# Performance work log

Measured on AMD Instinct MI355X. Metric: run time of the kernel, lower is better.

The kernel has to match this reference:

```python
import jax, jax.numpy as jnp
import numpy as np

D = 384      # d_model
H = 6        # num_heads
K = 8        # k_neighbors
B = 8        # batch
N = 2048     # num points
EPS = 1e-5


def _layer_norm(x, g, b):
    m = jnp.mean(x, axis=-1, keepdims=True)
    v = jnp.var(x, axis=-1, keepdims=True)
    return (x - m) * jax.lax.rsqrt(v + EPS) * g + b


def setup_inputs() -> dict:
    key = jax.random.key(0)
    ks = jax.random.split(key, 12)
    s = 0.02
    return {
        "coords": jax.random.normal(ks[0], (B, 3, N), jnp.float32),
        "features": jax.random.normal(ks[1], (B, D, N), jnp.float32),
        "ln1_g": jnp.ones((D,), jnp.float32),
        "ln1_b": jnp.zeros((D,), jnp.float32),
        "w_qkv": jax.random.normal(ks[2], (D, 3 * D), jnp.float32) * s,
        "w_attn_out": jax.random.normal(ks[3], (D, D), jnp.float32) * s,
        "b_attn_out": jnp.zeros((D,), jnp.float32),
        "ga_wq": jax.random.normal(ks[4], (D, D), jnp.float32) * s,
        "ga_wk": jax.random.normal(ks[5], (D, D), jnp.float32) * s,
        "ga_wv": jax.random.normal(ks[6], (D, D), jnp.float32) * s,
        "merge_w": jax.random.normal(ks[7], (2 * D, D), jnp.float32) * s,
        "merge_b": jnp.zeros((D,), jnp.float32),
        "ln2_g": jnp.ones((D,), jnp.float32),
        "ln2_b": jnp.zeros((D,), jnp.float32),
        "ff_w1": jax.random.normal(ks[8], (D, 2 * D), jnp.float32) * s,
        "ff_b1": jnp.zeros((2 * D,), jnp.float32),
        "ff_w2": jax.random.normal(ks[9], (2 * D, D), jnp.float32) * s,
        "ff_b2": jnp.zeros((D,), jnp.float32),
    }


def reference(coords, features, ln1_g, ln1_b, w_qkv, w_attn_out, b_attn_out,
              ga_wq, ga_wk, ga_wv, merge_w, merge_b, ln2_g, ln2_b,
              ff_w1, ff_b1, ff_w2, ff_b2):
    b, d, n = features.shape
    dh = d // H
    f = jnp.swapaxes(features, 1, 2)          # [B, N, D]
    nf = _layer_norm(f, ln1_g, ln1_b)         # [B, N, D]

    # --- dense multi-head self-attention branch ---
    qkv = nf @ w_qkv                           # [B, N, 3D]
    q, k, v = jnp.split(qkv, 3, axis=-1)
    def heads(x):
        return x.reshape(b, n, H, dh).transpose(0, 2, 1, 3)  # [B, H, N, dh]
    scores = jnp.einsum('bhqd,bhkd->bhqk', heads(q), heads(k)) / jnp.sqrt(jnp.float32(dh))
    attn = jnp.einsum('bhqk,bhkd->bhqd', jax.nn.softmax(scores, axis=-1), heads(v))
    attn = attn.transpose(0, 2, 1, 3).reshape(b, n, d)
    attn = attn @ w_attn_out + b_attn_out      # output projection

    # --- KNN graph-attention branch over normalized features ---
    c = jnp.swapaxes(coords, 1, 2)             # [B, N, 3]
    sq = jnp.sum(c * c, axis=-1)               # [B, N]
    d2 = sq[:, :, None] + sq[:, None, :] - 2.0 * jnp.einsum('bnd,bmd->bnm', c, c)
    _, idx = jax.lax.top_k(-d2, K)             # [B, N, K] nearest-neighbor indices
    nbrs = jax.vmap(lambda fe, i: fe[i])(nf, idx)  # [B, N, K, D]
    gq = nf @ ga_wq                             # [B, N, D]
    gk = nbrs @ ga_wk                           # [B, N, K, D]
    gv = nbrs @ ga_wv
    gs = jnp.einsum('bnd,bnkd->bnk', gq, gk) / jnp.sqrt(jnp.float32(d))
    geom = jnp.einsum('bnk,bnkd->bnd', jax.nn.softmax(gs, axis=-1), gv)  # [B, N, D]

    # --- merge + residual + FFN ---
    merged = jnp.concatenate([attn, geom], axis=-1) @ merge_w + merge_b
    f = f + merged
    h = _layer_norm(f, ln2_g, ln2_b)
    f = f + (jax.nn.gelu(h @ ff_w1 + ff_b1) @ ff_w2 + ff_b2)
    return jnp.swapaxes(f, 1, 2)               # [B, D, N]
```

## Files before the change

### kernel.cpp

```cpp
#include <hip/hip_runtime.h>
#include <hip/hip_bf16.h>
#include <cstdint>

#define D_MODEL 384
#define NHEAD 6
#define DHEAD 64
#define NPTS 2048
#define BATCH 8

typedef __attribute__((ext_vector_type(8))) short short8;
typedef __attribute__((ext_vector_type(4))) float floatx4;
typedef __attribute__((ext_vector_type(2))) unsigned int u32x2;
typedef __attribute__((ext_vector_type(4))) unsigned int u32x4;

__device__ __forceinline__ float bf2f(unsigned short u) {
    return __uint_as_float(((unsigned int)u) << 16);
}

__device__ __forceinline__ unsigned short f2bf(float f) {
    unsigned int u = __float_as_uint(f);
    unsigned int r = (u + 0x7FFFu + ((u >> 16) & 1u)) >> 16;
    return (unsigned short)r;
}

__device__ __forceinline__ unsigned cvtpk(float lo, float hi) {
    unsigned r;
    asm("v_cvt_pk_bf16_f32 %0, %1, %2" : "=v"(r) : "v"(lo), "v"(hi));
    return r;
}

#define TR16(dst, addr, imm) \
    asm volatile("ds_read_b64_tr_b16 %0, %1 offset:" #imm : "=v"(dst) : "v"(addr))

__device__ __forceinline__ float gelu_tanh(float x) {
    float x3 = x * x * x;
    return 0.5f * x * (1.0f + tanhf(0.7978845608028654f * (x + 0.044715f * x3)));
}

__device__ __forceinline__ void gload_lds16(const unsigned short* g, unsigned short* l) {
    __builtin_amdgcn_global_load_lds(
        (const __attribute__((address_space(1))) unsigned int*)g,
        (__attribute__((address_space(3))) unsigned int*)l, 16, 0, 0);
}

__global__ __launch_bounds__(256) void k_wprep(
    const float* __restrict__ wqkv, const float* __restrict__ wao,
    const float* __restrict__ wq, const float* __restrict__ wk,
    const float* __restrict__ wv, const float* __restrict__ wm,
    const float* __restrict__ w1, const float* __restrict__ w2,
    unsigned short* __restrict__ qkvT, unsigned short* __restrict__ aoT,
    unsigned short* __restrict__ gaT, unsigned short* __restrict__ mT,
    unsigned short* __restrict__ f1T, unsigned short* __restrict__ f2T) {
    __shared__ float tile[32][33];
    int id = blockIdx.x;
    const float* src;
    unsigned short* dst;
    int K, N;
    if (id < 432)       {            src = wqkv; dst = qkvT;            K = 384; N = 1152; }
    else if (id < 576)  { id -= 432; src = wao;  dst = aoT;             K = 384; N = 384; }
    else if (id < 720)  { id -= 576; src = wq;   dst = gaT;             K = 384; N = 384; }
    else if (id < 864)  { id -= 720; src = wk;   dst = gaT + 384 * 384; K = 384; N = 384; }
    else if (id < 1008) { id -= 864; src = wv;   dst = gaT + 768 * 384; K = 384; N = 384; }
    else if (id < 1296) { id -= 1008; src = wm;  dst = mT;              K = 768; N = 384; }
    else if (id < 1584) { id -= 1296; src = w1;  dst = f1T;             K = 384; N = 768; }
    else                { id -= 1584; src = w2;  dst = f2T;             K = 768; N = 384; }
    int ntiles = N >> 5;
    int nt = id % ntiles, kt = id / ntiles;
    int tx = threadIdx.x, ty = threadIdx.y;
#pragma unroll
    for (int i = 0; i < 32; i += 8)
        tile[ty + i][tx] = src[(size_t)(kt * 32 + ty + i) * N + nt * 32 + tx];
    __syncthreads();
#pragma unroll
    for (int i = 0; i < 32; i += 8)
        dst[(size_t)(nt * 32 + ty + i) * K + kt * 32 + tx] = f2bf(tile[tx][ty + i]);
}

__global__ __launch_bounds__(256) void k_transpose_in(const float* __restrict__ feat,
                                                      unsigned short* __restrict__ f) {
    __shared__ float tile[32][33];
    int b = blockIdx.z;
    int n0 = blockIdx.x * 32, d0 = blockIdx.y * 32;
    int tx = threadIdx.x, ty = threadIdx.y;
#pragma unroll
    for (int i = 0; i < 32; i += 8)
        tile[ty + i][tx] = feat[((size_t)b * D_MODEL + d0 + ty + i) * NPTS + n0 + tx];
    __syncthreads();
#pragma unroll
    for (int i = 0; i < 32; i += 8)
        f[((size_t)b * NPTS + n0 + ty + i) * D_MODEL + d0 + tx] = f2bf(tile[tx][ty + i]);
}

__global__ __launch_bounds__(256) void k_transpose_out(const unsigned short* __restrict__ f,
                                                       float* __restrict__ out) {
    __shared__ float tile[32][33];
    int b = blockIdx.z;
    int d0 = blockIdx.x * 32, n0 = blockIdx.y * 32;
    int tx = threadIdx.x, ty = threadIdx.y;
#pragma unroll
    for (int i = 0; i < 32; i += 8)
        tile[ty + i][tx] = bf2f(f[((size_t)b * NPTS + n0 + ty + i) * D_MODEL + d0 + tx]);
    __syncthreads();
#pragma unroll
    for (int i = 0; i < 32; i += 8)
        out[((size_t)b * D_MODEL + d0 + ty + i) * NPTS + n0 + tx] = tile[tx][ty + i];
}

__global__ __launch_bounds__(256) void k_vt(const unsigned short* __restrict__ qkv,
                                            unsigned short* __restrict__ vt) {
    __shared__ unsigned short tile[32][33];
    int b = blockIdx.z;
    int h = blockIdx.y >> 1, d0 = (blockIdx.y & 1) * 32;
    int n0 = blockIdx.x * 32;
    int tx = threadIdx.x, ty = threadIdx.y;
#pragma unroll
    for (int i = 0; i < 32; i += 8)
        tile[ty + i][tx] =
            qkv[((size_t)b * NPTS + n0 + ty + i) * 1152 + 768 + h * 64 + d0 + tx];
    __syncthreads();
#pragma unroll
    for (int i = 0; i < 32; i += 8)
        vt[(((size_t)(b * NHEAD + h) * 64) + d0 + ty + i) * NPTS + n0 + tx] = tile[tx][ty + i];
}

__global__ __launch_bounds__(128) void k_layernorm(const unsigned short* __restrict__ x,
                                                   const float* __restrict__ g,
                                                   const float* __restrict__ bt,
                                                   unsigned short* __restrict__ y) {
    int row = blockIdx.x, t = threadIdx.x;
    const unsigned short* xr = x + (size_t)row * D_MODEL;
    float v0 = bf2f(xr[t]), v1 = bf2f(xr[t + 128]), v2 = bf2f(xr[t + 256]);
    float s = v0 + v1 + v2;
    float s2 = v0 * v0 + v1 * v1 + v2 * v2;
#pragma unroll
    for (int off = 32; off > 0; off >>= 1) {
        s += __shfl_xor(s, off, 64);
        s2 += __shfl_xor(s2, off, 64);
    }
    __shared__ float ps[2], ps2[2];
    if ((t & 63) == 0) { ps[t >> 6] = s; ps2[t >> 6] = s2; }
    __syncthreads();
    s = ps[0] + ps[1];
    s2 = ps2[0] + ps2[1];
    float mean = s * (1.0f / 384.0f);
    float var = s2 * (1.0f / 384.0f) - mean * mean;
    var = fmaxf(var, 0.0f);
    float inv = 1.0f / sqrtf(var + 1e-5f);
    unsigned short* yr = y + (size_t)row * D_MODEL;
    yr[t]       = f2bf((v0 - mean) * inv * g[t]       + bt[t]);
    yr[t + 128] = f2bf((v1 - mean) * inv * g[t + 128] + bt[t + 128]);
    yr[t + 256] = f2bf((v2 - mean) * inv * g[t + 256] + bt[t + 256]);
}

__global__ __launch_bounds__(256) void k_knn(const float* __restrict__ coords,
                                             int* __restrict__ idx) {
    __shared__ float4 cpts[NPTS];
    __shared__ unsigned long long mbuf[32][8][8];
    int b = blockIdx.x >> 6;
    int n0 = (blockIdx.x & 63) * 32;
    const float* cb = coords + (size_t)b * 3 * NPTS;
    int tid = threadIdx.x;
#pragma unroll
    for (int i = 0; i < 8; i++) {
        int m = tid + i * 256;
        float x = cb[m], y = cb[NPTS + m], z = cb[2 * NPTS + m];
        float sq = __fadd_rn(__fadd_rn(__fmul_rn(x, x), __fmul_rn(y, y)), __fmul_rn(z, z));
        cpts[m] = make_float4(x, y, z, sq);
    }
    __syncthreads();
    int q = tid >> 3;
    int part = tid & 7;
    int n = n0 + q;
    float4 qp = cpts[n];
    float qx = qp.x, qy = qp.y, qz = qp.z, sqn = qp.w;
    unsigned long long heap[8];
#pragma unroll
    for (int k = 0; k < 8; k++) heap[k] = 0xFFFFFFFFFFFFFFFFull;
    for (int j = 0; j < 256; j++) {
        int m = j * 8 + part;
        float4 cp = cpts[m];
        float dot = __fadd_rn(__fadd_rn(__fmul_rn(qx, cp.x), __fmul_rn(qy, cp.y)),
                              __fmul_rn(qz, cp.z));
        float d2 = __fsub_rn(__fadd_rn(sqn, cp.w), __fmul_rn(2.0f, dot));
        unsigned int u = __float_as_uint(d2);
        u = (u & 0x80000000u) ? ~u : (u | 0x80000000u);
        unsigned long long key = ((unsigned long long)u << 32) | (unsigned int)m;
        if (key < heap[7]) {
            heap[7] = key;
#pragma unroll
            for (int t2 = 7; t2 > 0; t2--) {
                if (heap[t2] < heap[t2 - 1]) {
                    unsigned long long tmp = heap[t2];
                    heap[t2] = heap[t2 - 1];
                    heap[t2 - 1] = tmp;
                }
            }
        }
    }
#pragma unroll
    for (int k = 0; k < 8; k++) mbuf[q][part][k] = heap[k];
    __syncthreads();
    if (part == 0) {
        int p[8] = {0, 0, 0, 0, 0, 0, 0, 0};
        int* outr = idx + ((size_t)b * NPTS + n) * 8;
#pragma unroll
        for (int k = 0; k < 8; k++) {
            unsigned long long best = mbuf[q][0][p[0]];
            int bi = 0;
#pragma unroll
            for (int c = 1; c < 8; c++) {
                unsigned long long v = mbuf[q][c][p[c]];
                if (v < best) { best = v; bi = c; }
            }
            p[bi]++;
            outr[k] = (int)(best & 0xFFFFFFFFu);
        }
    }
}

__global__ __launch_bounds__(256) void k_gemm(const unsigned short* __restrict__ A, int lda,
                                              const unsigned short* __restrict__ WT,
                                              const float* __restrict__ bias,
                                              const unsigned short* __restrict__ res,
                                              unsigned short* __restrict__ C, int ldc,
                                              int K, int act) {
    __shared__ unsigned short Alds[2 * 128 * 32];
    __shared__ unsigned short Wlds[2 * 128 * 32];
    int tid = threadIdx.x;
    int wv = tid >> 6, lane = tid & 63;
    int l15 = lane & 15, quad = lane >> 4;
    int row0 = blockIdx.y * 128, col0 = blockIdx.x * 128;
    int wm = wv >> 1, wn = wv & 1;
    int wbase = tid & 192;
    floatx4 acc[4][4];
#pragma unroll
    for (int i = 0; i < 4; i++)
#pragma unroll
        for (int j = 0; j < 4; j++) acc[i][j] = (floatx4){0.f, 0.f, 0.f, 0.f};
    for (int k0 = 0; k0 < K; k0 += 64) {
#pragma unroll
        for (int i = 0; i < 4; i++) {
            int idx = i * 256 + tid;
            int kc = idx >> 9, row = (idx >> 2) & 127, ko = idx & 3;
            unsigned short* ldst = Alds + (size_t)(i * 256 + wbase) * 8;
            gload_lds16(A + (size_t)(row0 + row) * lda + k0 + kc * 32 + ko * 8, ldst);
            unsigned short* ldstw = Wlds + (size_t)(i * 256 + wbase) * 8;
            gload_lds16(WT + (size_t)(col0 + row) * K + k0 + kc * 32 + ko * 8, ldstw);
        }
        __syncthreads();
#pragma unroll
        for (int kc = 0; kc < 2; kc++) {
            short8 af[4], bf[4];
#pragma unroll
            for (int i = 0; i < 4; i++)
                af[i] = *(const short8*)&Alds[kc * 4096 + (wm * 64 + i * 16 + l15) * 32 + quad * 8];
#pragma unroll
            for (int j = 0; j < 4; j++)
                bf[j] = *(const short8*)&Wlds[kc * 4096 + (wn * 64 + j * 16 + l15) * 32 + quad * 8];
#pragma unroll
            for (int i = 0; i < 4; i++)
#pragma unroll
                for (int j = 0; j < 4; j++)
                    acc[i][j] =
                        __builtin_amdgcn_mfma_f32_16x16x32_bf16(bf[j], af[i], acc[i][j], 0, 0, 0);
        }
        __syncthreads();
    }
#pragma unroll
    for (int i = 0; i < 4; i++) {
        int r = row0 + wm * 64 + i * 16 + l15;
#pragma unroll
        for (int j = 0; j < 4; j++) {
            int cb = col0 + wn * 64 + j * 16 + quad * 4;
            float4 bv = bias ? *(const float4*)(bias + cb) : make_float4(0.f, 0.f, 0.f, 0.f);
            float v0 = acc[i][j][0] + bv.x;
            float v1 = acc[i][j][1] + bv.y;
            float v2 = acc[i][j][2] + bv.z;
            float v3 = acc[i][j][3] + bv.w;
            if (act == 1) {
                v0 = gelu_tanh(v0); v1 = gelu_tanh(v1);
                v2 = gelu_tanh(v2); v3 = gelu_tanh(v3);
            }
            if (res) {
                uint2 rv = *(const uint2*)(res + (size_t)r * ldc + cb);
                const unsigned short* rs = (const unsigned short*)&rv;
                v0 += bf2f(rs[0]); v1 += bf2f(rs[1]);
                v2 += bf2f(rs[2]); v3 += bf2f(rs[3]);
            }
            ushort4 u;
            u.x = f2bf(v0); u.y = f2bf(v1); u.z = f2bf(v2); u.w = f2bf(v3);
            *(ushort4*)(C + (size_t)r * ldc + cb) = u;
        }
    }
}

__global__ __launch_bounds__(256, 3) void k_attn(const unsigned short* __restrict__ qkv,
                                                 const unsigned short* __restrict__ vt,
                                                 unsigned short* __restrict__ attn) {
    __shared__ unsigned short Klds[2][64 * 64];
    __shared__ unsigned short VTl[2][64 * 64];
    __shared__ unsigned short Pt[4][2048];
    int b = blockIdx.z, h = blockIdx.y;
    int tid = threadIdx.x;
    int wv = tid >> 6, lane = tid & 63;
    int l15 = lane & 15, quad = lane >> 4;
    int qbase = blockIdx.x * 128 + wv * 32;
    const unsigned short* qkvb = qkv + (size_t)b * NPTS * 1152;
    const unsigned short* vtb = vt + (size_t)(b * NHEAD + h) * 64 * NPTS;
    const float SC = 0.18033688011112042f;
    short8 qf[2][2];
#pragma unroll
    for (int qt = 0; qt < 2; qt++) {
        const unsigned short* qptr =
            qkvb + (size_t)(qbase + qt * 16 + l15) * 1152 + h * 64 + quad * 8;
        qf[qt][0] = *(const short8*)qptr;
        qf[qt][1] = *(const short8*)(qptr + 32);
#pragma unroll
        for (int g = 0; g < 2; g++) {
            short8 v = qf[qt][g];
#pragma unroll
            for (int e = 0; e < 8; e++)
                v[e] = (short)f2bf(bf2f((unsigned short)v[e]) * SC);
            qf[qt][g] = v;
        }
    }
    short8 ones;
#pragma unroll
    for (int e = 0; e < 8; e++) ones[e] = (short)0x3F80;
    int x7 = l15 & 7;
    int sk0 = ((quad ^ x7) << 4);
    int sk1 = (((quad + 4) ^ x7) << 4);
    unsigned pa = (unsigned)(size_t)(__attribute__((address_space(3))) unsigned short*)&Pt[wv][0] +
                  (unsigned)(quad * 256 + l15 * 2);
    int sdg = tid & 7;
    floatx4 o[2][4];
#pragma unroll
    for (int qt = 0; qt < 2; qt++)
#pragma unroll
        for (int ct = 0; ct < 4; ct++) o[qt][ct] = (floatx4){0.f, 0.f, 0.f, 0.f};
    floatx4 l4[2];
    l4[0] = (floatx4){0.f, 0.f, 0.f, 0.f};
    l4[1] = (floatx4){0.f, 0.f, 0.f, 0.f};

    auto stage = [&](int c, int k0) {
#pragma unroll
        for (int i = 0; i < 2; i++) {
            int id = i * 256 + tid;
            int row = id >> 3;
            int sl = sdg ^ (row & 7);
            gload_lds16(qkvb + (size_t)(k0 + row) * 1152 + 384 + h * 64 + sl * 8,
                        &Klds[c][(size_t)(i * 256 + (tid & 192)) * 8]);
            gload_lds16(vtb + (size_t)row * NPTS + k0 + sl * 8,
                        &VTl[c][(size_t)(i * 256 + (tid & 192)) * 8]);
        }
    };

    stage(0, 0);
    __syncthreads();
    for (int t = 0; t < 32; ++t) {
        int c = t & 1;
        if (t < 31) stage(c ^ 1, (t + 1) * 64);
        const char* Kb = (const char*)&Klds[c][0];
        const char* Vb = (const char*)&VTl[c][0];
        short8 kf[4][2];
#pragma unroll
        for (int ct = 0; ct < 4; ct++) {
            kf[ct][0] = *(const short8*)(Kb + (ct * 16 + l15) * 128 + sk0);
            kf[ct][1] = *(const short8*)(Kb + (ct * 16 + l15) * 128 + sk1);
        }
#pragma unroll
        for (int qt = 0; qt < 2; qt++) {
            floatx4 s4[4];
#pragma unroll
            for (int ct = 0; ct < 4; ct++) {
                floatx4 z = (floatx4){0.f, 0.f, 0.f, 0.f};
                z = __builtin_amdgcn_mfma_f32_16x16x32_bf16(qf[qt][0], kf[ct][0], z, 0, 0, 0);
                z = __builtin_amdgcn_mfma_f32_16x16x32_bf16(qf[qt][1], kf[ct][1], z, 0, 0, 0);
                s4[ct] = z;
            }
#pragma unroll
            for (int ct = 0; ct < 4; ct++) {
                float p0 = __builtin_amdgcn_exp2f(s4[ct][0]);
                float p1 = __builtin_amdgcn_exp2f(s4[ct][1]);
                float p2 = __builtin_amdgcn_exp2f(s4[ct][2]);
                float p3 = __builtin_amdgcn_exp2f(s4[ct][3]);
                u32x2 pk;
                pk.x = cvtpk(p0, p1);
                pk.y = cvtpk(p2, p3);
                *(u32x2*)&Pt[wv][qt * 1024 + (ct * 16 + l15) * 16 + quad * 4] = pk;
            }
        }
        short8 vf[4][2];
#pragma unroll
        for (int ct = 0; ct < 4; ct++) {
            vf[ct][0] = *(const short8*)(Vb + (ct * 16 + l15) * 128 + sk0);
            vf[ct][1] = *(const short8*)(Vb + (ct * 16 + l15) * 128 + sk1);
        }
        asm volatile("s_waitcnt lgkmcnt(0)" ::: "memory");
        u32x2 q0g0l, q0g0h, q0g1l, q0g1h, q1g0l, q1g0h, q1g1l, q1g1h;
        TR16(q0g0l, pa, 0);
        TR16(q0g0h, pa, 128);
        TR16(q0g1l, pa, 1024);
        TR16(q0g1h, pa, 1152);
        TR16(q1g0l, pa, 2048);
        TR16(q1g0h, pa, 2176);
        TR16(q1g1l, pa, 3072);
        TR16(q1g1h, pa, 3200);
        asm volatile("s_waitcnt lgkmcnt(0)" ::: "memory");
        __builtin_amdgcn_sched_barrier(0);
        short8 pf[2][2];
        pf[0][0] = __builtin_bit_cast(short8, (u32x4){q0g0l.x, q0g0l.y, q0g0h.x, q0g0h.y});
        pf[0][1] = __builtin_bit_cast(short8, (u32x4){q0g1l.x, q0g1l.y, q0g1h.x, q0g1h.y});
        pf[1][0] = __builtin_bit_cast(short8, (u32x4){q1g0l.x, q1g0l.y, q1g0h.x, q1g0h.y});
        pf[1][1] = __builtin_bit_cast(short8, (u32x4){q1g1l.x, q1g1l.y, q1g1h.x, q1g1h.y});
#pragma unroll
        for (int ct = 0; ct < 4; ct++) {
#pragma unroll
            for (int qt = 0; qt < 2; qt++) {
                o[qt][ct] = __builtin_amdgcn_mfma_f32_16x16x32_bf16(vf[ct][0], pf[qt][0], o[qt][ct], 0, 0, 0);
                o[qt][ct] = __builtin_amdgcn_mfma_f32_16x16x32_bf16(vf[ct][1], pf[qt][1], o[qt][ct], 0, 0, 0);
            }
        }
#pragma unroll
        for (int qt = 0; qt < 2; qt++) {
            l4[qt] = __builtin_amdgcn_mfma_f32_16x16x32_bf16(ones, pf[qt][0], l4[qt], 0, 0, 0);
            l4[qt] = __builtin_amdgcn_mfma_f32_16x16x32_bf16(ones, pf[qt][1], l4[qt], 0, 0, 0);
        }
        if (t < 31) __syncthreads();
    }
#pragma unroll
    for (int qt = 0; qt < 2; qt++) {
        float linv = 1.0f / l4[qt][0];
#pragma unroll
        for (int ct = 0; ct < 4; ct++) {
            ushort4 u;
            u.x = f2bf(o[qt][ct][0] * linv);
            u.y = f2bf(o[qt][ct][1] * linv);
            u.z = f2bf(o[qt][ct][2] * linv);
            u.w = f2bf(o[qt][ct][3] * linv);
            *(ushort4*)(attn + ((size_t)b * NPTS + qbase + qt * 16 + l15) * 384 + h * 64 +
                        ct * 16 + quad * 4) = u;
        }
    }
}

__global__ __launch_bounds__(64) void k_geom(const unsigned short* __restrict__ gap,
                                             const int* __restrict__ idx,
                                             unsigned short* __restrict__ cat) {
    int r = blockIdx.x;
    int b = r >> 11;
    int t = threadIdx.x;
    int nb[8];
#pragma unroll
    for (int k = 0; k < 8; k++) nb[k] = idx[(size_t)r * 8 + k];
    const unsigned short* gqr = gap + (size_t)r * 1152;
    float qv[6];
#pragma unroll
    for (int j = 0; j < 6; j++) qv[j] = bf2f(gqr[t + 64 * j]);
    float s[8];
#pragma unroll
    for (int k = 0; k < 8; k++) {
        const unsigned short* nkr = gap + ((size_t)b * NPTS + nb[k]) * 1152 + 384;
        float acc = 0.0f;
#pragma unroll
        for (int j = 0; j < 6; j++) acc += qv[j] * bf2f(nkr[t + 64 * j]);
#pragma unroll
        for (int mm = 32; mm > 0; mm >>= 1) acc += __shfl_xor(acc, mm, 64);
        s[k] = acc * 0.05103103630798287f;
    }
    float mx = s[0];
#pragma unroll
    for (int k = 1; k < 8; k++) mx = fmaxf(mx, s[k]);
    float w[8];
    float sum = 0.0f;
#pragma unroll
    for (int k = 0; k < 8; k++) { w[k] = __expf(s[k] - mx); sum += w[k]; }
    float inv = 1.0f / sum;
    unsigned short* outr = cat + (size_t)r * 768 + 384;
#pragma unroll
    for (int j = 0; j < 6; j++) {
        int d = t + 64 * j;
        float acc = 0.0f;
#pragma unroll
        for (int k = 0; k < 8; k++)
            acc += w[k] * bf2f(gap[((size_t)b * NPTS + nb[k]) * 1152 + 768 + d]);
        outr[d] = f2bf(acc * inv);
    }
}

extern "C" void kernel_launch(void* const* d_in, const int* in_sizes, int n_in,
                              void* d_out, int out_size, void* d_ws, size_t ws_size,
                              hipStream_t stream) {
    (void)in_sizes; (void)n_in; (void)out_size; (void)ws_size;
    const float* coords     = (const float*)d_in[0];
    const float* features   = (const float*)d_in[1];
    const float* ln1_g      = (const float*)d_in[2];
    const float* ln1_b      = (const float*)d_in[3];
    const float* w_qkv      = (const float*)d_in[4];
    const float* w_attn_out = (const float*)d_in[5];
    const float* b_attn_out = (const float*)d_in[6];
    const float* ga_wq      = (const float*)d_in[7];
    const float* ga_wk      = (const float*)d_in[8];
    const float* ga_wv      = (const float*)d_in[9];
    const float* merge_w    = (const float*)d_in[10];
    const float* merge_b    = (const float*)d_in[11];
    const float* ln2_g      = (const float*)d_in[12];
    const float* ln2_b      = (const float*)d_in[13];
    const float* ff_w1      = (const float*)d_in[14];
    const float* ff_b1      = (const float*)d_in[15];
    const float* ff_w2      = (const float*)d_in[16];
    const float* ff_b2      = (const float*)d_in[17];

    unsigned short* W0 = (unsigned short*)d_ws;
    const size_t SZ = (size_t)BATCH * NPTS * D_MODEL;
    unsigned short* F    = W0 + 0 * SZ;
    unsigned short* NF   = W0 + 1 * SZ;
    unsigned short* QKV  = W0 + 2 * SZ;
    unsigned short* ATTN = W0 + 5 * SZ;
    unsigned short* VT   = W0 + 6 * SZ;
    unsigned short* CAT  = W0 + 2 * SZ;
    unsigned short* GAP  = W0 + 4 * SZ;
    unsigned short* F2   = W0 + 4 * SZ;
    unsigned short* HB   = W0 + 1 * SZ;
    unsigned short* T1   = W0 + 5 * SZ;
    unsigned short* FFIN = W0 + 2 * SZ;
    int*            IDX  = (int*)(W0 + 7 * SZ);
    unsigned short* WTS  = W0 + 7 * SZ + 262144;
    unsigned short* qkvT = WTS;
    unsigned short* aoT  = qkvT + 442368;
    unsigned short* gaT  = aoT + 147456;
    unsigned short* mT   = gaT + 442368;
    unsigned short* f1T  = mT + 294912;
    unsigned short* f2T  = f1T + 294912;

    const int M = BATCH * NPTS;

    k_wprep<<<1872, dim3(32, 8), 0, stream>>>(w_qkv, w_attn_out, ga_wq, ga_wk, ga_wv,
                                              merge_w, ff_w1, ff_w2,
                                              qkvT, aoT, gaT, mT, f1T, f2T);
    k_transpose_in<<<dim3(NPTS / 32, D_MODEL / 32, BATCH), dim3(32, 8), 0, stream>>>(features, F);
    k_layernorm<<<M, 128, 0, stream>>>(F, ln1_g, ln1_b, NF);
    k_knn<<<BATCH * (NPTS / 32), 256, 0, stream>>>(coords, IDX);
    k_gemm<<<dim3(9, M / 128), 256, 0, stream>>>(NF, 384, qkvT, nullptr, nullptr,
                                                 QKV, 1152, 384, 0);
    k_vt<<<dim3(NPTS / 32, 2 * NHEAD, BATCH), dim3(32, 8), 0, stream>>>(QKV, VT);
    k_attn<<<dim3(NPTS / 128, NHEAD, BATCH), 256, 0, stream>>>(QKV, VT, ATTN);
    k_gemm<<<dim3(3, M / 128), 256, 0, stream>>>(ATTN, 384, aoT, b_attn_out, nullptr,
                                                 CAT, 768, 384, 0);
    k_gemm<<<dim3(9, M / 128), 256, 0, stream>>>(NF, 384, gaT, nullptr, nullptr,
                                                 GAP, 1152, 384, 0);
    k_geom<<<M, 64, 0, stream>>>(GAP, IDX, CAT);
    k_gemm<<<dim3(3, M / 128), 256, 0, stream>>>(CAT, 768, mT, merge_b, F,
                                                 F2, 384, 768, 0);
    k_layernorm<<<M, 128, 0, stream>>>(F2, ln2_g, ln2_b, HB);
    k_gemm<<<dim3(6, M / 128), 256, 0, stream>>>(HB, 384, f1T, ff_b1, nullptr,
                                                 T1, 768, 384, 1);
    k_gemm<<<dim3(3, M / 128), 256, 0, stream>>>(T1, 768, f2T, ff_b2, F2,
                                                 FFIN, 384, 768, 0);
    k_transpose_out<<<dim3(D_MODEL / 32, NPTS / 32, BATCH), dim3(32, 8), 0, stream>>>(
        FFIN, (float*)d_out);
}
```

Before: 506.8 us.

## Assign one wavefront per KNN query with shuffle-based top-k merge

The KNN kernel now gives each query point a full 64-lane wavefront instead of 8 threads, so each lane scans 32 candidates rather than 256. The final top-8 is merged with wavefront xor-shuffle min-reductions instead of a shared-memory buffer and a serial single-thread merge. The sorted-insert loop is rewritten as a branchless compare-and-swap pass. The cost is 8x more blocks, each reloading all 2048 coordinates into LDS for only 4 queries, plus 8 rounds of 6-step 64-bit shuffle reductions.

```diff
diff --git a/kernel.cpp b/kernel.cpp
--- a/kernel.cpp
+++ b/kernel.cpp
@@ -155,9 +155,8 @@
 __global__ __launch_bounds__(256) void k_knn(const float* __restrict__ coords,
                                              int* __restrict__ idx) {
     __shared__ float4 cpts[NPTS];
-    __shared__ unsigned long long mbuf[32][8][8];
-    int b = blockIdx.x >> 6;
-    int n0 = (blockIdx.x & 63) * 32;
+    int b = blockIdx.x >> 9;
+    int q0 = (blockIdx.x & 511) * 4;
     const float* cb = coords + (size_t)b * 3 * NPTS;
     int tid = threadIdx.x;
 #pragma unroll
@@ -168,16 +167,15 @@
         cpts[m] = make_float4(x, y, z, sq);
     }
     __syncthreads();
-    int q = tid >> 3;
-    int part = tid & 7;
-    int n = n0 + q;
+    int wv = tid >> 6, lane = tid & 63;
+    int n = q0 + wv;
     float4 qp = cpts[n];
     float qx = qp.x, qy = qp.y, qz = qp.z, sqn = qp.w;
     unsigned long long heap[8];
 #pragma unroll
     for (int k = 0; k < 8; k++) heap[k] = 0xFFFFFFFFFFFFFFFFull;
-    for (int j = 0; j < 256; j++) {
-        int m = j * 8 + part;
+    for (int j = 0; j < 32; j++) {
+        int m = j * 64 + lane;
         float4 cp = cpts[m];
         float dot = __fadd_rn(__fadd_rn(__fmul_rn(qx, cp.x), __fmul_rn(qy, cp.y)),
                               __fmul_rn(qz, cp.z));
@@ -186,35 +184,38 @@
         u = (u & 0x80000000u) ? ~u : (u | 0x80000000u);
         unsigned long long key = ((unsigned long long)u << 32) | (unsigned int)m;
         if (key < heap[7]) {
-            heap[7] = key;
-#pragma unroll
-            for (int t2 = 7; t2 > 0; t2--) {
-                if (heap[t2] < heap[t2 - 1]) {
-                    unsigned long long tmp = heap[t2];
-                    heap[t2] = heap[t2 - 1];
-                    heap[t2 - 1] = tmp;
-                }
+            unsigned long long cur = key;
+#pragma unroll
+            for (int t2 = 0; t2 < 8; t2++) {
+                unsigned long long h = heap[t2];
+                unsigned long long lo = h < cur ? h : cur;
+                cur = h < cur ? cur : h;
+                heap[t2] = lo;
             }
         }
     }
-#pragma unroll
-    for (int k = 0; k < 8; k++) mbuf[q][part][k] = heap[k];
-    __syncthreads();
-    if (part == 0) {
-        int p[8] = {0, 0, 0, 0, 0, 0, 0, 0};
-        int* outr = idx + ((size_t)b * NPTS + n) * 8;
-#pragma unroll
-        for (int k = 0; k < 8; k++) {
-            unsigned long long best = mbuf[q][0][p[0]];
-            int bi = 0;
-#pragma unroll
-            for (int c = 1; c < 8; c++) {
-                unsigned long long v = mbuf[q][c][p[c]];
-                if (v < best) { best = v; bi = c; }
-            }
-            p[bi]++;
-            outr[k] = (int)(best & 0xFFFFFFFFu);
-        }
+    unsigned long long cur = heap[0];
+    unsigned int out[8];
+#pragma unroll
+    for (int r = 0; r < 8; r++) {
+        unsigned long long w = cur;
+#pragma unroll
+        for (int off = 1; off < 64; off <<= 1) {
+            unsigned long long o = __shfl_xor(w, off, 64);
+            w = o < w ? o : w;
+        }
+        out[r] = (unsigned int)(w & 0xFFFFFFFFu);
+        if (cur == w) {
+#pragma unroll
+            for (int t2 = 0; t2 < 7; t2++) heap[t2] = heap[t2 + 1];
+            heap[7] = 0xFFFFFFFFFFFFFFFFull;
+            cur = heap[0];
+        }
+    }
+    if (lane == 0) {
+        unsigned int* outr = (unsigned int*)(idx + ((size_t)b * NPTS + n) * 8);
+        *(uint4*)outr = make_uint4(out[0], out[1], out[2], out[3]);
+        *(uint4*)(outr + 4) = make_uint4(out[4], out[5], out[6], out[7]);
     }
 }
 
@@ -540,7 +541,7 @@
                                               qkvT, aoT, gaT, mT, f1T, f2T);
     k_transpose_in<<<dim3(NPTS / 32, D_MODEL / 32, BATCH), dim3(32, 8), 0, stream>>>(features, F);
     k_layernorm<<<M, 128, 0, stream>>>(F, ln1_g, ln1_b, NF);
-    k_knn<<<BATCH * (NPTS / 32), 256, 0, stream>>>(coords, IDX);
+    k_knn<<<BATCH * (NPTS / 4), 256, 0, stream>>>(coords, IDX);
     k_gemm<<<dim3(9, M / 128), 256, 0, stream>>>(NF, 384, qkvT, nullptr, nullptr,
                                                  QKV, 1152, 384, 0);
     k_vt<<<dim3(NPTS / 32, 2 * NHEAD, BATCH), dim3(32, 8), 0, stream>>>(QKV, VT);
```

Result: faster. 480.7 us (-5.1%).
